# Kernel tuning notes

Hardware: AMD Instinct MI355X
Metric: run time of the kernel (lower is better)

## Reference

```python
import jax, jax.numpy as jnp
import numpy as np

B, S, D = 32, 8192, 64


def setup_inputs() -> dict:
    key = jax.random.key(0)
    k1, k2 = jax.random.split(key)
    input_real = jax.random.normal(k1, (B, S, D), dtype=jnp.float32)
    input_imag = jax.random.normal(k2, (B, S, D), dtype=jnp.float32)
    return {"input_real": input_real, "input_imag": input_imag}


def reference(input_real, input_imag):
    # ComplexMixture: mean over seq of per-token complex outer products v v^H.
    # Original builds [B,S,D,D] via 4 batch_dots then means over S; fused here
    # as Gram contractions over the sequence axis (no [B,S,D,D] intermediate).
    seq_len = input_real.shape[1]
    inv_s = jnp.asarray(1.0 / seq_len, dtype=input_real.dtype)
    rr = jnp.einsum('bsi,bsj->bij', input_real, input_real)
    ii = jnp.einsum('bsi,bsj->bij', input_imag, input_imag)
    ri = jnp.einsum('bsi,bsj->bij', input_real, input_imag)
    out_real = (rr + ii) * inv_s                     # [B, D, D], symmetric
    out_imag = (ri - jnp.swapaxes(ri, 1, 2)) * inv_s  # [B, D, D], antisymmetric
    return (out_real, out_imag)
```

## Files before the change

### kernel.cpp

```cpp
#include <hip/hip_runtime.h>


#define BATCH 32
#define SEQ   8192
#define DD    64
#define BK    128

typedef __bf16 bf16x8 __attribute__((ext_vector_type(8)));
typedef float  f32x16 __attribute__((ext_vector_type(16)));
typedef float  f32x4  __attribute__((ext_vector_type(4)));

__device__ __forceinline__ unsigned bf16pk(float a, float b) {
  unsigned ua = __builtin_bit_cast(unsigned, a);
  unsigned ub = __builtin_bit_cast(unsigned, b);
  ua = (ua + 0x7fffu + ((ua >> 16) & 1u)) >> 16;
  ub = (ub + 0x7fffu + ((ub >> 16) & 1u)) >> 16;
  return (ua & 0xffffu) | (ub << 16);
}

__device__ __forceinline__ int permd(int d) {
  return d ^ ((d >> 3) & 1) ^ (((d >> 4) & 1) << 1);
}

template<int CHUNKS>
__global__ __launch_bounds__(256, 2) void gram_partial(
    const float* __restrict__ R, const float* __restrict__ I,
    float* __restrict__ ws)
{
  constexpr int SCHUNK = SEQ / CHUNKS;
  constexpr int NIT    = SCHUNK / BK;
  __shared__ uint4 lds[2][32][64];
  const int tid  = threadIdx.x;
  const int wave = tid >> 6;
  const int lane = tid & 63;
  const int b = blockIdx.x & 31;
  const int c = blockIdx.x >> 5;
  const float* Rb = R + (size_t)b * (SEQ * DD);
  const float* Ib = I + (size_t)b * (SEQ * DD);
  const int m0  = (wave >> 1) * 32;
  const int n0  = (wave & 1) * 32;
  const int l31 = lane & 31;
  const int lhi = lane >> 5;
  const int g   = tid >> 4;
  const int q   = tid & 15;
  const int pa  = permd(m0 + l31);
  const int pb  = permd(n0 + l31);
  int pw[4];
  #pragma unroll
  for (int cc = 0; cc < 4; ++cc) pw[cc] = permd(q * 4 + cc);

  f32x16 accR = {};
  f32x16 accI = {};
  const int chunk0 = c * SCHUNK;

  f32x4 rv[8], iv[8];

#define LOADT(it_) do { \
    const size_t sb_ = (size_t)(chunk0 + (it_) * BK + g * 8); \
    const f32x4* pR_ = (const f32x4*)(Rb + sb_ * DD) + q; \
    const f32x4* pI_ = (const f32x4*)(Ib + sb_ * DD) + q; \
    _Pragma("unroll") \
    for (int j = 0; j < 8; ++j) { rv[j] = pR_[j * 16]; iv[j] = pI_[j * 16]; } \
    asm volatile("" ::: "memory"); \
  } while (0)

#define PACKW(buf_) do { \
    _Pragma("unroll") \
    for (int cc = 0; cc < 4; ++cc) { \
      uint4 qR_, qI_; \
      qR_.x = bf16pk(rv[0][cc], rv[1][cc]); qR_.y = bf16pk(rv[2][cc], rv[3][cc]); \
      qR_.z = bf16pk(rv[4][cc], rv[5][cc]); qR_.w = bf16pk(rv[6][cc], rv[7][cc]); \
      qI_.x = bf16pk(iv[0][cc], iv[1][cc]); qI_.y = bf16pk(iv[2][cc], iv[3][cc]); \
      qI_.z = bf16pk(iv[4][cc], iv[5][cc]); qI_.w = bf16pk(iv[6][cc], iv[7][cc]); \
      lds[buf_][g][pw[cc]]      = qR_; \
      lds[buf_][16 + g][pw[cc]] = qI_; \
    } \
  } while (0)

#define TILEBAR() do { \
    __builtin_amdgcn_sched_barrier(0); \
    asm volatile("s_waitcnt lgkmcnt(0)" ::: "memory"); \
    __builtin_amdgcn_s_barrier(); \
    __builtin_amdgcn_sched_barrier(0); \
  } while (0)

  LOADT(0);
  PACKW(0);
  TILEBAR();

  #pragma unroll
  for (int it = 0; it < NIT; ++it) {
    const int buf = it & 1;
    if (it + 1 < NIT) LOADT(it + 1);
    #pragma unroll
    for (int ks = 0; ks < BK / 16; ++ks) {
      const int kg = ks * 2 + lhi;
      bf16x8 aR = __builtin_bit_cast(bf16x8, lds[buf][kg][pa]);
      bf16x8 bR = __builtin_bit_cast(bf16x8, lds[buf][kg][pb]);
      bf16x8 aI = __builtin_bit_cast(bf16x8, lds[buf][16 + kg][pa]);
      bf16x8 bI = __builtin_bit_cast(bf16x8, lds[buf][16 + kg][pb]);
      accR = __builtin_amdgcn_mfma_f32_32x32x16_bf16(aR, bR, accR, 0, 0, 0);
      accR = __builtin_amdgcn_mfma_f32_32x32x16_bf16(aI, bI, accR, 0, 0, 0);
      accI = __builtin_amdgcn_mfma_f32_32x32x16_bf16(aR, bI, accI, 0, 0, 0);
    }
    if (it + 1 < NIT) {
      PACKW(buf ^ 1);
      TILEBAR();
    }
  }
#undef LOADT
#undef PACKW
#undef TILEBAR

  float* wsR = ws + ((size_t)(c * 32 + b) * 2) * 4096;
  float* wsM = wsR + 4096;
  const int jj = n0 + l31;
  #pragma unroll
  for (int r = 0; r < 16; ++r) {
    const int i = m0 + (r & 3) + 8 * (r >> 2) + 4 * lhi;
    wsR[i * 64 + jj] = accR[r];
  }
  float* ldsf = (float*)lds;
  #pragma unroll
  for (int r = 0; r < 16; ++r) {
    const int i = m0 + (r & 3) + 8 * (r >> 2) + 4 * lhi;
    ldsf[i * 65 + jj] = accI[r];
  }
  __syncthreads();
  #pragma unroll
  for (int k = 0; k < 16; ++k) {
    const int e = tid + 256 * k;
    const int i = e >> 6, j = e & 63;
    wsM[e] = ldsf[i * 65 + j] - ldsf[j * 65 + i];
  }
}

template<int CHUNKS>
__global__ __launch_bounds__(256) void gram_reduce(
    const float4* __restrict__ ws, float4* __restrict__ out)
{
  const int o = blockIdx.x * 256 + threadIdx.x;
  const int kind = o >> 15;
  const int rem  = o & 32767;
  const int b    = rem >> 10;
  const int e    = rem & 1023;
  const float inv = 1.0f / (float)SEQ;
  float sx = 0.f, sy = 0.f, sz = 0.f, sw = 0.f;
  #pragma unroll
  for (int cc = 0; cc < CHUNKS; ++cc) {
    float4 v = ws[((size_t)(cc * 32 + b) * 2 + kind) * 1024 + e];
    sx += v.x; sy += v.y; sz += v.z; sw += v.w;
  }
  float4 r; r.x = sx * inv; r.y = sy * inv; r.z = sz * inv; r.w = sw * inv;
  out[o] = r;
}

extern "C" void kernel_launch(void* const* d_in, const int* in_sizes, int n_in,
                              void* d_out, int out_size, void* d_ws, size_t ws_size,
                              hipStream_t stream) {
  const float* R = (const float*)d_in[0];
  const float* I = (const float*)d_in[1];
  float* out = (float*)d_out;
  float* ws  = (float*)d_ws;

  const size_t need16 = (size_t)16 * 32 * 2 * 4096 * 4;
  if (ws_size >= need16) {
    gram_partial<16><<<BATCH * 16, 256, 0, stream>>>(R, I, ws);
    gram_reduce<16><<<256, 256, 0, stream>>>((const float4*)ws, (float4*)out);
  } else {
    gram_partial<8><<<BATCH * 8, 256, 0, stream>>>(R, I, ws);
    gram_reduce<8><<<256, 256, 0, stream>>>((const float4*)ws, (float4*)out);
  }
}
```

Measured before the change: 154.3 us.

## Fuse partial Gram and reduction via per-wave sequence split and atomics

Each wave now handles its own slice of the sequence chunk and computes the full 64x64 Gram blocks with private LDS staging, so the per-tile block barriers go away. Only the upper triangular blocks of the symmetric real part are computed, which trims the MFMA count. The four waves' partial results are combined in LDS, scaled, and atomically added into the output after a memset, replacing the separate workspace reduce kernel. The cost is more accumulator registers, float atomics with nondeterministic summation order, and an extra memset launch.

```diff
diff --git a/kernel.cpp b/kernel.cpp
--- a/kernel.cpp
+++ b/kernel.cpp
@@ -1,10 +1,13 @@
 #include <hip/hip_runtime.h>
 
 
-#define BATCH 32
-#define SEQ   8192
-#define DD    64
-#define BK    128
+#define BATCH  32
+#define SEQ    8192
+#define DD     64
+#define CHUNKS 16
+#define SCHUNK (SEQ / CHUNKS)
+#define WROWS  (SCHUNK / 4)
+#define NST    (WROWS / 32)
 
 typedef __bf16 bf16x8 __attribute__((ext_vector_type(8)));
 typedef float  f32x16 __attribute__((ext_vector_type(16)));
@@ -22,43 +25,41 @@
   return d ^ ((d >> 3) & 1) ^ (((d >> 4) & 1) << 1);
 }
 
-template<int CHUNKS>
-__global__ __launch_bounds__(256, 2) void gram_partial(
+__device__ __forceinline__ void atomAdd(float* p, float v) {
+  __hip_atomic_fetch_add(p, v, __ATOMIC_RELAXED, __HIP_MEMORY_SCOPE_AGENT);
+}
+
+__global__ __launch_bounds__(256, 2) void gram_fused(
     const float* __restrict__ R, const float* __restrict__ I,
-    float* __restrict__ ws)
+    float* __restrict__ out)
 {
-  constexpr int SCHUNK = SEQ / CHUNKS;
-  constexpr int NIT    = SCHUNK / BK;
-  __shared__ uint4 lds[2][32][64];
+  __shared__ uint4 stg[4][2][2][4][64];
   const int tid  = threadIdx.x;
-  const int wave = tid >> 6;
+  const int w    = tid >> 6;
   const int lane = tid & 63;
+  const int l31  = lane & 31;
+  const int lhi  = lane >> 5;
+  const int g4   = lane >> 4;
+  const int q    = lane & 15;
   const int b = blockIdx.x & 31;
   const int c = blockIdx.x >> 5;
   const float* Rb = R + (size_t)b * (SEQ * DD);
   const float* Ib = I + (size_t)b * (SEQ * DD);
-  const int m0  = (wave >> 1) * 32;
-  const int n0  = (wave & 1) * 32;
-  const int l31 = lane & 31;
-  const int lhi = lane >> 5;
-  const int g   = tid >> 4;
-  const int q   = tid & 15;
-  const int pa  = permd(m0 + l31);
-  const int pb  = permd(n0 + l31);
+  const int p0 = permd(l31);
+  const int p1 = permd(32 + l31);
   int pw[4];
   #pragma unroll
   for (int cc = 0; cc < 4; ++cc) pw[cc] = permd(q * 4 + cc);
 
-  f32x16 accR = {};
-  f32x16 accI = {};
-  const int chunk0 = c * SCHUNK;
+  f32x16 r00 = {}, r01 = {}, r11 = {};
+  f32x16 i00 = {}, i01 = {}, i10 = {}, i11 = {};
 
   f32x4 rv[8], iv[8];
+  const size_t rbase = (size_t)(c * SCHUNK + w * WROWS + g4 * 8) * DD;
 
-#define LOADT(it_) do { \
-    const size_t sb_ = (size_t)(chunk0 + (it_) * BK + g * 8); \
-    const f32x4* pR_ = (const f32x4*)(Rb + sb_ * DD) + q; \
-    const f32x4* pI_ = (const f32x4*)(Ib + sb_ * DD) + q; \
+#define LOADT(st_) do { \
+    const f32x4* pR_ = (const f32x4*)(Rb + rbase + (size_t)(st_) * 32 * DD) + q; \
+    const f32x4* pI_ = (const f32x4*)(Ib + rbase + (size_t)(st_) * 32 * DD) + q; \
     _Pragma("unroll") \
     for (int j = 0; j < 8; ++j) { rv[j] = pR_[j * 16]; iv[j] = pI_[j * 16]; } \
     asm volatile("" ::: "memory"); \
@@ -72,87 +73,107 @@
       qR_.z = bf16pk(rv[4][cc], rv[5][cc]); qR_.w = bf16pk(rv[6][cc], rv[7][cc]); \
       qI_.x = bf16pk(iv[0][cc], iv[1][cc]); qI_.y = bf16pk(iv[2][cc], iv[3][cc]); \
       qI_.z = bf16pk(iv[4][cc], iv[5][cc]); qI_.w = bf16pk(iv[6][cc], iv[7][cc]); \
-      lds[buf_][g][pw[cc]]      = qR_; \
-      lds[buf_][16 + g][pw[cc]] = qI_; \
+      stg[w][buf_][0][g4][pw[cc]] = qR_; \
+      stg[w][buf_][1][g4][pw[cc]] = qI_; \
     } \
-  } while (0)
-
-#define TILEBAR() do { \
-    __builtin_amdgcn_sched_barrier(0); \
-    asm volatile("s_waitcnt lgkmcnt(0)" ::: "memory"); \
-    __builtin_amdgcn_s_barrier(); \
-    __builtin_amdgcn_sched_barrier(0); \
   } while (0)
 
   LOADT(0);
   PACKW(0);
-  TILEBAR();
 
   #pragma unroll
-  for (int it = 0; it < NIT; ++it) {
-    const int buf = it & 1;
-    if (it + 1 < NIT) LOADT(it + 1);
+  for (int st = 0; st < NST; ++st) {
+    const int buf = st & 1;
+    if (st + 1 < NST) LOADT(st + 1);
     #pragma unroll
-    for (int ks = 0; ks < BK / 16; ++ks) {
+    for (int ks = 0; ks < 2; ++ks) {
       const int kg = ks * 2 + lhi;
-      bf16x8 aR = __builtin_bit_cast(bf16x8, lds[buf][kg][pa]);
-      bf16x8 bR = __builtin_bit_cast(bf16x8, lds[buf][kg][pb]);
-      bf16x8 aI = __builtin_bit_cast(bf16x8, lds[buf][16 + kg][pa]);
-      bf16x8 bI = __builtin_bit_cast(bf16x8, lds[buf][16 + kg][pb]);
-      accR = __builtin_amdgcn_mfma_f32_32x32x16_bf16(aR, bR, accR, 0, 0, 0);
-      accR = __builtin_amdgcn_mfma_f32_32x32x16_bf16(aI, bI, accR, 0, 0, 0);
-      accI = __builtin_amdgcn_mfma_f32_32x32x16_bf16(aR, bI, accI, 0, 0, 0);
+      bf16x8 fR0 = __builtin_bit_cast(bf16x8, stg[w][buf][0][kg][p0]);
+      bf16x8 fR1 = __builtin_bit_cast(bf16x8, stg[w][buf][0][kg][p1]);
+      bf16x8 fI0 = __builtin_bit_cast(bf16x8, stg[w][buf][1][kg][p0]);
+      bf16x8 fI1 = __builtin_bit_cast(bf16x8, stg[w][buf][1][kg][p1]);
+      r00 = __builtin_amdgcn_mfma_f32_32x32x16_bf16(fR0, fR0, r00, 0, 0, 0);
+      r01 = __builtin_amdgcn_mfma_f32_32x32x16_bf16(fR0, fR1, r01, 0, 0, 0);
+      r11 = __builtin_amdgcn_mfma_f32_32x32x16_bf16(fR1, fR1, r11, 0, 0, 0);
+      i00 = __builtin_amdgcn_mfma_f32_32x32x16_bf16(fR0, fI0, i00, 0, 0, 0);
+      i01 = __builtin_amdgcn_mfma_f32_32x32x16_bf16(fR0, fI1, i01, 0, 0, 0);
+      i10 = __builtin_amdgcn_mfma_f32_32x32x16_bf16(fR1, fI0, i10, 0, 0, 0);
+      i11 = __builtin_amdgcn_mfma_f32_32x32x16_bf16(fR1, fI1, i11, 0, 0, 0);
+      r00 = __builtin_amdgcn_mfma_f32_32x32x16_bf16(fI0, fI0, r00, 0, 0, 0);
+      r01 = __builtin_amdgcn_mfma_f32_32x32x16_bf16(fI0, fI1, r01, 0, 0, 0);
+      r11 = __builtin_amdgcn_mfma_f32_32x32x16_bf16(fI1, fI1, r11, 0, 0, 0);
     }
-    if (it + 1 < NIT) {
-      PACKW(buf ^ 1);
-      TILEBAR();
-    }
+    if (st + 1 < NST) PACKW(buf ^ 1);
   }
 #undef LOADT
 #undef PACKW
-#undef TILEBAR
 
-  float* wsR = ws + ((size_t)(c * 32 + b) * 2) * 4096;
-  float* wsM = wsR + 4096;
-  const int jj = n0 + l31;
+  __syncthreads();
+  float* sc = (float*)stg;
+  const float inv = 1.0f / (float)SEQ;
+  float* outR = out + (size_t)b * 4096;
+  float* outM = out + 131072 + (size_t)b * 4096;
+
+#define WRQ(stride_, t_, acc_) do { \
+    _Pragma("unroll") \
+    for (int r = 0; r < 16; ++r) { \
+      const int p_ = (r & 3) + 8 * (r >> 2) + 4 * lhi; \
+      sc[w * (stride_) + (t_) * 1056 + p_ * 33 + l31] = acc_[r]; \
+    } \
+  } while (0)
+
+  WRQ(3176, 0, r00); WRQ(3176, 1, r01); WRQ(3176, 2, r11);
+  __syncthreads();
   #pragma unroll
-  for (int r = 0; r < 16; ++r) {
-    const int i = m0 + (r & 3) + 8 * (r >> 2) + 4 * lhi;
-    wsR[i * 64 + jj] = accR[r];
-  }
-  float* ldsf = (float*)lds;
-  #pragma unroll
-  for (int r = 0; r < 16; ++r) {
-    const int i = m0 + (r & 3) + 8 * (r >> 2) + 4 * lhi;
-    ldsf[i * 65 + jj] = accI[r];
+  for (int kk = 0; kk < 12; ++kk) {
+    const int e = tid + 256 * kk;
+    const int t = e >> 10, idx = e & 1023, p = idx >> 5, qq = idx & 31;
+    float v = 0.f;
+    #pragma unroll
+    for (int wv = 0; wv < 4; ++wv) v += sc[wv * 3176 + t * 1056 + p * 33 + qq];
+    v *= inv;
+    if (t == 0)      atomAdd(&outR[p * 64 + qq], v);
+    else if (t == 1) { atomAdd(&outR[p * 64 + 32 + qq], v);
+                       atomAdd(&outR[(32 + qq) * 64 + p], v); }
+    else             atomAdd(&outR[(32 + p) * 64 + 32 + qq], v);
   }
   __syncthreads();
+
+  WRQ(2120, 0, i01); WRQ(2120, 1, i10);
+  __syncthreads();
   #pragma unroll
-  for (int k = 0; k < 16; ++k) {
-    const int e = tid + 256 * k;
-    const int i = e >> 6, j = e & 63;
-    wsM[e] = ldsf[i * 65 + j] - ldsf[j * 65 + i];
+  for (int kk = 0; kk < 4; ++kk) {
+    const int e = tid + 256 * kk;
+    const int p = e >> 5, qq = e & 31;
+    float v01 = 0.f, v10 = 0.f;
+    #pragma unroll
+    for (int wv = 0; wv < 4; ++wv) {
+      v01 += sc[wv * 2120 + 0 * 1056 + p * 33 + qq];
+      v10 += sc[wv * 2120 + 1 * 1056 + qq * 33 + p];
+    }
+    const float m = (v01 - v10) * inv;
+    atomAdd(&outM[p * 64 + 32 + qq],  m);
+    atomAdd(&outM[(32 + qq) * 64 + p], -m);
   }
-}
+  __syncthreads();
 
-template<int CHUNKS>
-__global__ __launch_bounds__(256) void gram_reduce(
-    const float4* __restrict__ ws, float4* __restrict__ out)
-{
-  const int o = blockIdx.x * 256 + threadIdx.x;
-  const int kind = o >> 15;
-  const int rem  = o & 32767;
-  const int b    = rem >> 10;
-  const int e    = rem & 1023;
-  const float inv = 1.0f / (float)SEQ;
-  float sx = 0.f, sy = 0.f, sz = 0.f, sw = 0.f;
+  WRQ(2120, 0, i00); WRQ(2120, 1, i11);
+  __syncthreads();
   #pragma unroll
-  for (int cc = 0; cc < CHUNKS; ++cc) {
-    float4 v = ws[((size_t)(cc * 32 + b) * 2 + kind) * 1024 + e];
-    sx += v.x; sy += v.y; sz += v.z; sw += v.w;
+  for (int kk = 0; kk < 8; ++kk) {
+    const int e = tid + 256 * kk;
+    const int t = e >> 10, idx = e & 1023, p = idx >> 5, qq = idx & 31;
+    float a = 0.f, bt = 0.f;
+    #pragma unroll
+    for (int wv = 0; wv < 4; ++wv) {
+      a  += sc[wv * 2120 + t * 1056 + p * 33 + qq];
+      bt += sc[wv * 2120 + t * 1056 + qq * 33 + p];
+    }
+    const float m = (a - bt) * inv;
+    if (t == 0) atomAdd(&outM[p * 64 + qq], m);
+    else        atomAdd(&outM[(32 + p) * 64 + 32 + qq], m);
   }
-  float4 r; r.x = sx * inv; r.y = sy * inv; r.z = sz * inv; r.w = sw * inv;
-  out[o] = r;
+#undef WRQ
 }
 
 extern "C" void kernel_launch(void* const* d_in, const int* in_sizes, int n_in,
@@ -161,14 +182,8 @@
   const float* R = (const float*)d_in[0];
   const float* I = (const float*)d_in[1];
   float* out = (float*)d_out;
-  float* ws  = (float*)d_ws;
+  (void)d_ws; (void)ws_size;
 
-  const size_t need16 = (size_t)16 * 32 * 2 * 4096 * 4;
-  if (ws_size >= need16) {
-    gram_partial<16><<<BATCH * 16, 256, 0, stream>>>(R, I, ws);
-    gram_reduce<16><<<256, 256, 0, stream>>>((const float4*)ws, (float4*)out);
-  } else {
-    gram_partial<8><<<BATCH * 8, 256, 0, stream>>>(R, I, ws);
-    gram_reduce<8><<<256, 256, 0, stream>>>((const float4*)ws, (float4*)out);
-  }
+  hipMemsetAsync(d_out, 0, (size_t)out_size, stream);
+  gram_fused<<<BATCH * CHUNKS, 256, 0, stream>>>(R, I, out);
 }
```

Result: slower. 200.4 us (+29.9%).

## Fuse partial Gram and reduction via atomics, split R/I loads across half-blocks

Applied to the files above, without the earlier changes.

Replaces the two-kernel partial-sum plus reduce scheme with a single kernel that atomically adds scaled partial Gram tiles straight into the zeroed output, removing the workspace round trip and the second launch. It doubles the sequence chunks to 32 per batch (1024 blocks), shrinks the tile to 64 rows, and has half of each block load the real input and half the imaginary one, which lowers register pressure to allow 4 blocks per CU. In exchange it adds a memset launch and contended float atomics (32 per output element), and the summation order is no longer deterministic.

```diff
diff --git a/kernel.cpp b/kernel.cpp
--- a/kernel.cpp
+++ b/kernel.cpp
@@ -1,10 +1,13 @@
 #include <hip/hip_runtime.h>
 
 
-#define BATCH 32
-#define SEQ   8192
-#define DD    64
-#define BK    128
+#define BATCH  32
+#define SEQ    8192
+#define DD     64
+#define CHUNKS 32
+#define SCHUNK (SEQ / CHUNKS)
+#define TR     64
+#define NIT    (SCHUNK / TR)
 
 typedef __bf16 bf16x8 __attribute__((ext_vector_type(8)));
 typedef float  f32x16 __attribute__((ext_vector_type(16)));
@@ -22,58 +25,54 @@
   return d ^ ((d >> 3) & 1) ^ (((d >> 4) & 1) << 1);
 }
 
-template<int CHUNKS>
-__global__ __launch_bounds__(256, 2) void gram_partial(
+__device__ __forceinline__ void atomAdd(float* p, float v) {
+  __hip_atomic_fetch_add(p, v, __ATOMIC_RELAXED, __HIP_MEMORY_SCOPE_AGENT);
+}
+
+__global__ __launch_bounds__(256, 4) void gram_fused(
     const float* __restrict__ R, const float* __restrict__ I,
-    float* __restrict__ ws)
+    float* __restrict__ out)
 {
-  constexpr int SCHUNK = SEQ / CHUNKS;
-  constexpr int NIT    = SCHUNK / BK;
-  __shared__ uint4 lds[2][32][64];
+  __shared__ uint4 lds[2][2][8][64];
   const int tid  = threadIdx.x;
   const int wave = tid >> 6;
   const int lane = tid & 63;
+  const int l31  = lane & 31;
+  const int lhi  = lane >> 5;
+  const int mat  = tid >> 7;
+  const int g    = (tid >> 4) & 7;
+  const int q    = tid & 15;
   const int b = blockIdx.x & 31;
   const int c = blockIdx.x >> 5;
-  const float* Rb = R + (size_t)b * (SEQ * DD);
-  const float* Ib = I + (size_t)b * (SEQ * DD);
-  const int m0  = (wave >> 1) * 32;
-  const int n0  = (wave & 1) * 32;
-  const int l31 = lane & 31;
-  const int lhi = lane >> 5;
-  const int g   = tid >> 4;
-  const int q   = tid & 15;
-  const int pa  = permd(m0 + l31);
-  const int pb  = permd(n0 + l31);
+  const float* Mb = (mat ? I : R) + (size_t)b * (SEQ * DD);
+  const int m0 = (wave >> 1) * 32;
+  const int n0 = (wave & 1) * 32;
+  const int pa = permd(m0 + l31);
+  const int pb = permd(n0 + l31);
   int pw[4];
   #pragma unroll
   for (int cc = 0; cc < 4; ++cc) pw[cc] = permd(q * 4 + cc);
 
   f32x16 accR = {};
   f32x16 accI = {};
-  const int chunk0 = c * SCHUNK;
 
-  f32x4 rv[8], iv[8];
+  f32x4 v[8];
+  const size_t rbase = (size_t)(c * SCHUNK + g * 8) * DD;
 
-#define LOADT(it_) do { \
-    const size_t sb_ = (size_t)(chunk0 + (it_) * BK + g * 8); \
-    const f32x4* pR_ = (const f32x4*)(Rb + sb_ * DD) + q; \
-    const f32x4* pI_ = (const f32x4*)(Ib + sb_ * DD) + q; \
+#define LOADT(t_) do { \
+    const f32x4* p_ = (const f32x4*)(Mb + rbase + (size_t)(t_) * TR * DD) + q; \
     _Pragma("unroll") \
-    for (int j = 0; j < 8; ++j) { rv[j] = pR_[j * 16]; iv[j] = pI_[j * 16]; } \
+    for (int j = 0; j < 8; ++j) v[j] = p_[j * 16]; \
     asm volatile("" ::: "memory"); \
   } while (0)
 
 #define PACKW(buf_) do { \
     _Pragma("unroll") \
     for (int cc = 0; cc < 4; ++cc) { \
-      uint4 qR_, qI_; \
-      qR_.x = bf16pk(rv[0][cc], rv[1][cc]); qR_.y = bf16pk(rv[2][cc], rv[3][cc]); \
-      qR_.z = bf16pk(rv[4][cc], rv[5][cc]); qR_.w = bf16pk(rv[6][cc], rv[7][cc]); \
-      qI_.x = bf16pk(iv[0][cc], iv[1][cc]); qI_.y = bf16pk(iv[2][cc], iv[3][cc]); \
-      qI_.z = bf16pk(iv[4][cc], iv[5][cc]); qI_.w = bf16pk(iv[6][cc], iv[7][cc]); \
-      lds[buf_][g][pw[cc]]      = qR_; \
-      lds[buf_][16 + g][pw[cc]] = qI_; \
+      uint4 u_; \
+      u_.x = bf16pk(v[0][cc], v[1][cc]); u_.y = bf16pk(v[2][cc], v[3][cc]); \
+      u_.z = bf16pk(v[4][cc], v[5][cc]); u_.w = bf16pk(v[6][cc], v[7][cc]); \
+      lds[buf_][mat][g][pw[cc]] = u_; \
     } \
   } while (0)
 
@@ -93,12 +92,12 @@
     const int buf = it & 1;
     if (it + 1 < NIT) LOADT(it + 1);
     #pragma unroll
-    for (int ks = 0; ks < BK / 16; ++ks) {
+    for (int ks = 0; ks < TR / 16; ++ks) {
       const int kg = ks * 2 + lhi;
-      bf16x8 aR = __builtin_bit_cast(bf16x8, lds[buf][kg][pa]);
-      bf16x8 bR = __builtin_bit_cast(bf16x8, lds[buf][kg][pb]);
-      bf16x8 aI = __builtin_bit_cast(bf16x8, lds[buf][16 + kg][pa]);
-      bf16x8 bI = __builtin_bit_cast(bf16x8, lds[buf][16 + kg][pb]);
+      bf16x8 aR = __builtin_bit_cast(bf16x8, lds[buf][0][kg][pa]);
+      bf16x8 bR = __builtin_bit_cast(bf16x8, lds[buf][0][kg][pb]);
+      bf16x8 aI = __builtin_bit_cast(bf16x8, lds[buf][1][kg][pa]);
+      bf16x8 bI = __builtin_bit_cast(bf16x8, lds[buf][1][kg][pb]);
       accR = __builtin_amdgcn_mfma_f32_32x32x16_bf16(aR, bR, accR, 0, 0, 0);
       accR = __builtin_amdgcn_mfma_f32_32x32x16_bf16(aI, bI, accR, 0, 0, 0);
       accI = __builtin_amdgcn_mfma_f32_32x32x16_bf16(aR, bI, accI, 0, 0, 0);
@@ -112,47 +111,31 @@
 #undef PACKW
 #undef TILEBAR
 
-  float* wsR = ws + ((size_t)(c * 32 + b) * 2) * 4096;
-  float* wsM = wsR + 4096;
+  const float inv = 1.0f / (float)SEQ;
+  float* outR = out + (size_t)b * 4096;
+  float* outM = out + 131072 + (size_t)b * 4096;
   const int jj = n0 + l31;
+
   #pragma unroll
   for (int r = 0; r < 16; ++r) {
     const int i = m0 + (r & 3) + 8 * (r >> 2) + 4 * lhi;
-    wsR[i * 64 + jj] = accR[r];
+    atomAdd(&outR[i * 64 + jj], accR[r] * inv);
   }
-  float* ldsf = (float*)lds;
+
+  __syncthreads();
+  float* sc = (float*)lds;
   #pragma unroll
   for (int r = 0; r < 16; ++r) {
     const int i = m0 + (r & 3) + 8 * (r >> 2) + 4 * lhi;
-    ldsf[i * 65 + jj] = accI[r];
+    sc[i * 65 + jj] = accI[r];
   }
   __syncthreads();
   #pragma unroll
-  for (int k = 0; k < 16; ++k) {
-    const int e = tid + 256 * k;
-    const int i = e >> 6, j = e & 63;
-    wsM[e] = ldsf[i * 65 + j] - ldsf[j * 65 + i];
+  for (int r = 0; r < 16; ++r) {
+    const int i = m0 + (r & 3) + 8 * (r >> 2) + 4 * lhi;
+    const float m = (sc[i * 65 + jj] - sc[jj * 65 + i]) * inv;
+    atomAdd(&outM[i * 64 + jj], m);
   }
-}
-
-template<int CHUNKS>
-__global__ __launch_bounds__(256) void gram_reduce(
-    const float4* __restrict__ ws, float4* __restrict__ out)
-{
-  const int o = blockIdx.x * 256 + threadIdx.x;
-  const int kind = o >> 15;
-  const int rem  = o & 32767;
-  const int b    = rem >> 10;
-  const int e    = rem & 1023;
-  const float inv = 1.0f / (float)SEQ;
-  float sx = 0.f, sy = 0.f, sz = 0.f, sw = 0.f;
-  #pragma unroll
-  for (int cc = 0; cc < CHUNKS; ++cc) {
-    float4 v = ws[((size_t)(cc * 32 + b) * 2 + kind) * 1024 + e];
-    sx += v.x; sy += v.y; sz += v.z; sw += v.w;
-  }
-  float4 r; r.x = sx * inv; r.y = sy * inv; r.z = sz * inv; r.w = sw * inv;
-  out[o] = r;
 }
 
 extern "C" void kernel_launch(void* const* d_in, const int* in_sizes, int n_in,
@@ -161,14 +144,8 @@
   const float* R = (const float*)d_in[0];
   const float* I = (const float*)d_in[1];
   float* out = (float*)d_out;
-  float* ws  = (float*)d_ws;
+  (void)d_ws; (void)ws_size;
 
-  const size_t need16 = (size_t)16 * 32 * 2 * 4096 * 4;
-  if (ws_size >= need16) {
-    gram_partial<16><<<BATCH * 16, 256, 0, stream>>>(R, I, ws);
-    gram_reduce<16><<<256, 256, 0, stream>>>((const float4*)ws, (float4*)out);
-  } else {
-    gram_partial<8><<<BATCH * 8, 256, 0, stream>>>(R, I, ws);
-    gram_reduce<8><<<256, 256, 0, stream>>>((const float4*)ws, (float4*)out);
-  }
+  hipMemsetAsync(d_out, 0, (size_t)out_size, stream);
+  gram_fused<<<BATCH * CHUNKS, 256, 0, stream>>>(R, I, out);
 }
```

Result: slower. 158.3 us (+2.6%).
